# Kernel tuning notes

Measured on AMD Instinct MI355X. Metric: run time of the kernel, lower is better.

Reference implementation:

```python
import jax, jax.numpy as jnp
import numpy as np

NUM_HEADS = 6
KERNEL = 5
EPS = 1e-6


def _neighbor_idx(L, k):
    # NATTEN neighborhood: window start clamped so every query has exactly k neighbors
    starts = jnp.clip(jnp.arange(L) - k // 2, 0, L - k)
    return starts[:, None] + jnp.arange(k)  # [L, k]


def ada_rmsnorm(x, scale, w1, b1, w2, b2):
    # x: [B,C,D,H,W]; RMS over spatial dims, gamma from channel means via small MLP
    rms = jnp.sqrt(jnp.mean(x * x, axis=(2, 3, 4), keepdims=True) + EPS)
    xn = x / rms
    stats = jnp.mean(x, axis=(2, 3, 4))                 # [B,C]
    h = jax.nn.relu(stats @ w1.T + b1)                  # [B,2C]
    gamma = jax.nn.sigmoid(h @ w2.T + b2)               # [B,C]
    return xn * (scale * gamma[:, :, None, None, None])


def reference(x, scale1, n1_w1, n1_b1, n1_w2, n1_b2,
              qkv_w, qkv_b, proj_w, proj_b,
              scale2, n2_w1, n2_b1, n2_w2, n2_b2,
              mlp_w1, mlp_b1, mlp_w2, mlp_b2):
    B, C, D, H, W = x.shape
    nh_, k_ = NUM_HEADS, KERNEL
    hd = C // nh_
    K3 = k_ ** 3

    # --- norm1 + neighborhood attention ---
    h = ada_rmsnorm(x, scale1, n1_w1, n1_b1, n1_w2, n1_b2)
    t = jnp.transpose(h, (0, 2, 3, 4, 1))               # [B,D,H,W,C]
    qkv = t @ qkv_w.T + qkv_b                           # [B,D,H,W,3C]
    q, k, v = jnp.split(qkv, 3, axis=-1)
    q = q.reshape(B, D, H, W, nh_, hd)
    k = k.reshape(B, D, H, W, nh_, hd)
    v = v.reshape(B, D, H, W, nh_, hd)

    iD = _neighbor_idx(D, k_)
    iH = _neighbor_idx(H, k_)
    iW = _neighbor_idx(W, k_)
    nd = iD[:, None, None, :, None, None]               # [D,1,1,k,1,1]
    nhh = iH[None, :, None, None, :, None]              # [1,H,1,1,k,1]
    nw = iW[None, None, :, None, None, :]               # [1,1,W,1,1,k]

    k_nb = k[:, nd, nhh, nw].reshape(B, D, H, W, K3, nh_, hd)
    v_nb = v[:, nd, nhh, nw].reshape(B, D, H, W, K3, nh_, hd)

    scale_qk = hd ** -0.5
    scores = jnp.einsum('bdhwnc,bdhwknc->bdhwnk', q, k_nb) * scale_qk  # [B,D,H,W,heads,K3]
    p = jax.nn.softmax(scores, axis=-1)
    o = jnp.einsum('bdhwnk,bdhwknc->bdhwnc', p, v_nb).reshape(B, D, H, W, C)
    o = o @ proj_w.T + proj_b                            # output projection
    x = x + jnp.transpose(o, (0, 4, 1, 2, 3))

    # --- norm2 + 1x1-conv MLP (GELU exact) ---
    h2 = ada_rmsnorm(x, scale2, n2_w1, n2_b1, n2_w2, n2_b2)
    m = jnp.einsum('oc,bcdhw->bodhw', mlp_w1, h2) + mlp_b1[None, :, None, None, None]
    m = jax.nn.gelu(m, approximate=False)
    m = jnp.einsum('oc,bcdhw->bodhw', mlp_w2, m) + mlp_b2[None, :, None, None, None]
    return x + m


def setup_inputs() -> dict:
    key = jax.random.key(0)
    ks = jax.random.split(key, 16)
    B, C, D, H, W = 1, 192, 16, 16, 16
    hid = 2 * C
    mlp_h = int(4.0 * C)
    s = 0.02
    inp = {
        'x': jax.random.normal(ks[0], (B, C, D, H, W), jnp.float32),
        'scale1': jnp.ones((1, C, 1, 1, 1), jnp.float32),
        'n1_w1': jax.random.normal(ks[1], (hid, C), jnp.float32) * s,
        'n1_b1': jnp.zeros((hid,), jnp.float32),
        'n1_w2': jax.random.normal(ks[2], (C, hid), jnp.float32) * s,
        'n1_b2': jnp.zeros((C,), jnp.float32),
        'qkv_w': jax.random.normal(ks[3], (3 * C, C), jnp.float32) * s,
        'qkv_b': jnp.zeros((3 * C,), jnp.float32),
        'proj_w': jax.random.normal(ks[4], (C, C), jnp.float32) * s,
        'proj_b': jnp.zeros((C,), jnp.float32),
        'scale2': jnp.ones((1, C, 1, 1, 1), jnp.float32),
        'n2_w1': jax.random.normal(ks[5], (hid, C), jnp.float32) * s,
        'n2_b1': jnp.zeros((hid,), jnp.float32),
        'n2_w2': jax.random.normal(ks[6], (C, hid), jnp.float32) * s,
        'n2_b2': jnp.zeros((C,), jnp.float32),
        'mlp_w1': jax.random.normal(ks[7], (mlp_h, C), jnp.float32) * s,
        'mlp_b1': jnp.zeros((mlp_h,), jnp.float32),
        'mlp_w2': jax.random.normal(ks[8], (C, mlp_h), jnp.float32) * s,
        'mlp_b2': jnp.zeros((C,), jnp.float32),
    }
    return inp
```

## Files before the change

kernel.cpp:

```cpp
#include <hip/hip_runtime.h>
#include <hip/hip_bf16.h>
#include <cmath>


#define NPOS 4096
#define C_CH 192

typedef __bf16 bf16x8 __attribute__((ext_vector_type(8)));
typedef __bf16 bf16x4 __attribute__((ext_vector_type(4)));
typedef float  f32x4  __attribute__((ext_vector_type(4)));

__global__ __launch_bounds__(256) void prep_kernel(
    const float* __restrict__ s0, const float* __restrict__ s1,
    const float* __restrict__ s2, const float* __restrict__ s3,
    __bf16* __restrict__ d0, __bf16* __restrict__ d1,
    __bf16* __restrict__ d2, __bf16* __restrict__ d3,
    const float* __restrict__ x, float* __restrict__ sums, float* __restrict__ sumsq)
{
    int b = blockIdx.x;
    if (b < 432) {
        const float* src; __bf16* dst; int base;
        if (b < 108)      { src = s0; dst = d0; base = b; }
        else if (b < 144) { src = s1; dst = d1; base = b - 108; }
        else if (b < 288) { src = s2; dst = d2; base = b - 144; }
        else              { src = s3; dst = d3; base = b - 288; }
        int i = (base * 256 + threadIdx.x) * 4;
        float4 v = *(const float4*)(src + i);
        bf16x4 o = { (__bf16)v.x, (__bf16)v.y, (__bf16)v.z, (__bf16)v.w };
        *(bf16x4*)(dst + i) = o;
        return;
    }
    int c = b - 432;
    const float4* xc = (const float4*)(x + (size_t)c * NPOS);
    float a = 0.f, a2 = 0.f;
    for (int i = threadIdx.x; i < NPOS / 4; i += 256) {
        float4 v = xc[i];
        a  += v.x + v.y + v.z + v.w;
        a2 += v.x * v.x + v.y * v.y + v.z * v.z + v.w * v.w;
    }
    #pragma unroll
    for (int off = 32; off > 0; off >>= 1) {
        a  += __shfl_down(a, off);
        a2 += __shfl_down(a2, off);
    }
    __shared__ float ls[4], ls2[4];
    int wid = threadIdx.x >> 6;
    if ((threadIdx.x & 63) == 0) { ls[wid] = a; ls2[wid] = a2; }
    __syncthreads();
    if (threadIdx.x == 0) {
        float t = 0.f, t2 = 0.f;
        #pragma unroll
        for (int w = 0; w < 4; w++) { t += ls[w]; t2 += ls2[w]; }
        sums[c] = t; sumsq[c] = t2;
    }
}

__global__ __launch_bounds__(256) void stats_kernel(
    const float* __restrict__ x, float* __restrict__ sums, float* __restrict__ sumsq)
{
    int c = blockIdx.x;
    const float4* xc = (const float4*)(x + (size_t)c * NPOS);
    float a = 0.f, a2 = 0.f;
    for (int i = threadIdx.x; i < NPOS / 4; i += 256) {
        float4 v = xc[i];
        a  += v.x + v.y + v.z + v.w;
        a2 += v.x * v.x + v.y * v.y + v.z * v.z + v.w * v.w;
    }
    #pragma unroll
    for (int off = 32; off > 0; off >>= 1) {
        a  += __shfl_down(a, off);
        a2 += __shfl_down(a2, off);
    }
    __shared__ float ls[4], ls2[4];
    int wid = threadIdx.x >> 6;
    if ((threadIdx.x & 63) == 0) { ls[wid] = a; ls2[wid] = a2; }
    __syncthreads();
    if (threadIdx.x == 0) {
        float t = 0.f, t2 = 0.f;
        #pragma unroll
        for (int w = 0; w < 4; w++) { t += ls[w]; t2 += ls2[w]; }
        sums[c] = t; sumsq[c] = t2;
    }
}

__global__ __launch_bounds__(256) void convx_kernel(
    const float* __restrict__ x,
    const float* __restrict__ sums, const float* __restrict__ sumsq,
    const float* __restrict__ scale,
    const float* __restrict__ w1, const float* __restrict__ b1,
    const float* __restrict__ w2, const float* __restrict__ b2,
    __bf16* __restrict__ xb)
{
    __shared__ float stats[C_CH];
    __shared__ float h[384];
    __shared__ float gsl[C_CH];
    __shared__ float lds[192 * 65];
    int t = threadIdx.x;

    if (t < C_CH) stats[t] = sums[t] * (1.0f / (float)NPOS);
    __syncthreads();
    for (int j = t; j < 384; j += 256) {
        float acc = b1[j];
        const float* wr = w1 + (size_t)j * C_CH;
        #pragma unroll 4
        for (int c = 0; c < C_CH; c += 4) {
            float4 w4 = *(const float4*)(wr + c);
            acc += w4.x * stats[c] + w4.y * stats[c + 1] + w4.z * stats[c + 2] + w4.w * stats[c + 3];
        }
        h[j] = fmaxf(acc, 0.0f);
    }
    __syncthreads();
    if (t < C_CH) {
        float acc = b2[t];
        const float* wr = w2 + (size_t)t * 384;
        #pragma unroll 4
        for (int j = 0; j < 384; j += 4) {
            float4 w4 = *(const float4*)(wr + j);
            acc += w4.x * h[j] + w4.y * h[j + 1] + w4.z * h[j + 2] + w4.w * h[j + 3];
        }
        float g = 1.0f / (1.0f + __expf(-acc));
        float rms = sqrtf(sumsq[t] * (1.0f / (float)NPOS) + 1e-6f);
        gsl[t] = scale[t] * g / rms;
    }
    __syncthreads();

    int p0 = blockIdx.x * 64;
    for (int idx = t; idx < 192 * 16; idx += 256) {
        int row = idx >> 4, p4 = idx & 15;
        float4 v = *(const float4*)(x + (size_t)row * NPOS + p0 + p4 * 4);
        float g = gsl[row];
        lds[row * 65 + p4 * 4 + 0] = v.x * g;
        lds[row * 65 + p4 * 4 + 1] = v.y * g;
        lds[row * 65 + p4 * 4 + 2] = v.z * g;
        lds[row * 65 + p4 * 4 + 3] = v.w * g;
    }
    __syncthreads();
    for (int idx = t; idx < 48 * 64; idx += 256) {
        int c4 = idx >> 6, p = idx & 63;
        bf16x4 o;
        #pragma unroll
        for (int j = 0; j < 4; j++) o[j] = (__bf16)lds[(c4 * 4 + j) * 65 + p];
        *(bf16x4*)(xb + (size_t)(p0 + p) * 192 + c4 * 4) = o;
    }
}

template <int K, int EPI, int CFG>
__global__ __launch_bounds__(256) void mfma_gemm(
    const __bf16* __restrict__ W, const float* __restrict__ bias,
    const __bf16* __restrict__ X, void* __restrict__ out,
    const float* __restrict__ resid, int M,
    __bf16* __restrict__ out_kv)
{
    constexpr int MT = 2;
    constexpr int NT = (CFG == 1) ? 2 : 1;
    constexpr int BM = (CFG == 1) ? 64 : 32;
    constexpr int BN = 64;
    int lane = threadIdx.x & 63;
    int wv   = threadIdx.x >> 6;
    int r16  = lane & 15;
    int quad = lane >> 4;
    int wvm = (CFG == 1) ? (wv >> 1) : 0;
    int wvn = (CFG == 1) ? (wv & 1) : wv;
    int mBase = blockIdx.y * BM + wvm * 32;
    int nBase = blockIdx.x * BN + wvn * (NT * 16);

    f32x4 acc[MT][NT];
    #pragma unroll
    for (int i = 0; i < MT; i++)
        #pragma unroll
        for (int j = 0; j < NT; j++)
            acc[i][j] = (f32x4){0.f, 0.f, 0.f, 0.f};

    const __bf16* wp = W + (size_t)(mBase + r16) * K + quad * 8;
    const __bf16* xp = X + (size_t)(nBase + r16) * K + quad * 8;

    #pragma unroll 6
    for (int ks = 0; ks < K / 32; ks++) {
        bf16x8 a[MT], b[NT];
        #pragma unroll
        for (int rt = 0; rt < MT; rt++)
            a[rt] = *(const bf16x8*)(wp + (size_t)rt * 16 * K + ks * 32);
        #pragma unroll
        for (int ct = 0; ct < NT; ct++)
            b[ct] = *(const bf16x8*)(xp + (size_t)ct * 16 * K + ks * 32);
        #pragma unroll
        for (int rt = 0; rt < MT; rt++)
            #pragma unroll
            for (int ct = 0; ct < NT; ct++)
                acc[rt][ct] = __builtin_amdgcn_mfma_f32_16x16x32_bf16(a[rt], b[ct], acc[rt][ct], 0, 0, 0);
    }

    #pragma unroll
    for (int rt = 0; rt < MT; rt++) {
        int m0 = mBase + rt * 16 + quad * 4;
        float b0 = bias[m0], b1 = bias[m0 + 1], b2 = bias[m0 + 2], b3 = bias[m0 + 3];
        #pragma unroll
        for (int ct = 0; ct < NT; ct++) {
            int n = nBase + ct * 16 + r16;
            f32x4 a4 = acc[rt][ct];
            float g0 = a4[0] + b0, g1 = a4[1] + b1, g2 = a4[2] + b2, g3 = a4[3] + b3;
            if (EPI == 0) {
                int sect = m0 / 192;
                int o0 = m0 - sect * 192;
                if (sect == 0) {
                    const float qs = 0.17677669529663687f;
                    *(float4*)((float*)out + (size_t)n * 192 + o0) =
                        make_float4(g0 * qs, g1 * qs, g2 * qs, g3 * qs);
                } else {
                    bf16x4 v = { (__bf16)g0, (__bf16)g1, (__bf16)g2, (__bf16)g3 };
                    *(bf16x4*)(out_kv + (size_t)n * 384 + (sect - 1) * 192 + o0) = v;
                }
            } else if (EPI == 2) {
                float* o = (float*)out;
                size_t i0 = (size_t)m0 * NPOS + n;
                o[i0]            = g0 + resid[i0];
                o[i0 + NPOS]     = g1 + resid[i0 + NPOS];
                o[i0 + 2 * NPOS] = g2 + resid[i0 + 2 * NPOS];
                o[i0 + 3 * NPOS] = g3 + resid[i0 + 3 * NPOS];
            } else {
                bf16x4 v;
                v[0] = (__bf16)(0.5f * g0 * (1.0f + erff(g0 * 0.7071067811865475f)));
                v[1] = (__bf16)(0.5f * g1 * (1.0f + erff(g1 * 0.7071067811865475f)));
                v[2] = (__bf16)(0.5f * g2 * (1.0f + erff(g2 * 0.7071067811865475f)));
                v[3] = (__bf16)(0.5f * g3 * (1.0f + erff(g3 * 0.7071067811865475f)));
                *(bf16x4*)((__bf16*)out + (size_t)n * M + m0) = v;
            }
        }
    }
}

__global__ __launch_bounds__(256) void attn_kernel(
    const float* __restrict__ q, const __bf16* __restrict__ kv, __bf16* __restrict__ o)
{
    int t = threadIdx.x;
    int pairIdx = blockIdx.x * 8 + (t >> 5);
    int sg   = (t >> 3) & 3;
    int lane = t & 7;
    int pos = pairIdx / 6;
    int head = pairIdx - pos * 6;
    int wq = pos & 15;
    int hq = (pos >> 4) & 15;
    int dq = pos >> 8;
    int d0 = min(max(dq - 2, 0), 11);
    int h0 = min(max(hq - 2, 0), 11);
    int w0 = min(max(wq - 2, 0), 11);

    const __bf16* kvb = kv + head * 32 + lane * 4;
    float4 q4 = *(const float4*)(q + (size_t)pos * 192 + head * 32 + lane * 4);

    float l = 0.0f;
    float4 acc = make_float4(0.f, 0.f, 0.f, 0.f);

    for (int dh = sg; dh < 25; dh += 4) {
        int di = dh / 5;
        int hi = dh - di * 5;
        int np0 = (d0 + di) * 256 + (h0 + hi) * 16 + w0;
        const __bf16* p = kvb + (size_t)np0 * 384;
        #pragma unroll
        for (int wi = 0; wi < 5; wi++) {
            uint2 kk = *(const uint2*)p;
            uint2 vv = *(const uint2*)(p + 192);
            float k0 = __uint_as_float(kk.x << 16);
            float k1 = __uint_as_float(kk.x & 0xFFFF0000u);
            float k2 = __uint_as_float(kk.y << 16);
            float k3 = __uint_as_float(kk.y & 0xFFFF0000u);
            float s = q4.x * k0 + q4.y * k1 + q4.z * k2 + q4.w * k3;
            s += __shfl_xor(s, 1);
            s += __shfl_xor(s, 2);
            s += __shfl_xor(s, 4);
            float pr = __expf(s);
            l += pr;
            acc.x += pr * __uint_as_float(vv.x << 16);
            acc.y += pr * __uint_as_float(vv.x & 0xFFFF0000u);
            acc.z += pr * __uint_as_float(vv.y << 16);
            acc.w += pr * __uint_as_float(vv.y & 0xFFFF0000u);
            p += 384;
        }
    }

    #pragma unroll
    for (int off = 8; off <= 16; off <<= 1) {
        l     += __shfl_xor(l, off);
        acc.x += __shfl_xor(acc.x, off);
        acc.y += __shfl_xor(acc.y, off);
        acc.z += __shfl_xor(acc.z, off);
        acc.w += __shfl_xor(acc.w, off);
    }

    if (sg == 0) {
        float rl = 1.0f / l;
        bf16x4 ov = { (__bf16)(acc.x * rl), (__bf16)(acc.y * rl),
                      (__bf16)(acc.z * rl), (__bf16)(acc.w * rl) };
        *(bf16x4*)(o + (size_t)pos * 192 + head * 32 + lane * 4) = ov;
    }
}

extern "C" void kernel_launch(void* const* d_in, const int* in_sizes, int n_in,
                              void* d_out, int out_size, void* d_ws, size_t ws_size,
                              hipStream_t stream)
{
    const float* x      = (const float*)d_in[0];
    const float* scale1 = (const float*)d_in[1];
    const float* n1_w1  = (const float*)d_in[2];
    const float* n1_b1  = (const float*)d_in[3];
    const float* n1_w2  = (const float*)d_in[4];
    const float* n1_b2  = (const float*)d_in[5];
    const float* qkv_w  = (const float*)d_in[6];
    const float* qkv_b  = (const float*)d_in[7];
    const float* proj_w = (const float*)d_in[8];
    const float* proj_b = (const float*)d_in[9];
    const float* scale2 = (const float*)d_in[10];
    const float* n2_w1  = (const float*)d_in[11];
    const float* n2_b1  = (const float*)d_in[12];
    const float* n2_w2  = (const float*)d_in[13];
    const float* n2_b2  = (const float*)d_in[14];
    const float* mlp_w1 = (const float*)d_in[15];
    const float* mlp_b1 = (const float*)d_in[16];
    const float* mlp_w2 = (const float*)d_in[17];
    const float* mlp_b2 = (const float*)d_in[18];

    float* ws = (float*)d_ws;
    float*  q_buf  = ws;
    __bf16* kv_buf = (__bf16*)(ws + 786432);
    __bf16* m_buf  = (__bf16*)ws;
    __bf16* xb     = (__bf16*)(ws + 2359296);
    __bf16* o_attn = (__bf16*)(ws + 2752512);
    __bf16* qkv_wb = (__bf16*)(ws + 3145728);
    __bf16* proj_wb = qkv_wb + 110592;
    __bf16* m1_wb   = proj_wb + 36864;
    __bf16* m2_wb   = m1_wb + 147456;
    float*  sums   = ws + 3366912;
    float*  sumsq  = sums + 192;

    float* x2 = (float*)d_out;

    prep_kernel<<<624, 256, 0, stream>>>(qkv_w, proj_w, mlp_w1, mlp_w2,
                                         qkv_wb, proj_wb, m1_wb, m2_wb,
                                         x, sums, sumsq);
    convx_kernel<<<64, 256, 0, stream>>>(x, sums, sumsq, scale1,
                                         n1_w1, n1_b1, n1_w2, n1_b2, xb);
    mfma_gemm<192, 0, 1><<<dim3(64, 9), 256, 0, stream>>>(qkv_wb, qkv_b, xb, (void*)q_buf, nullptr, 576, kv_buf);
    attn_kernel<<<3072, 256, 0, stream>>>(q_buf, kv_buf, o_attn);
    mfma_gemm<192, 2, 2><<<dim3(64, 6), 256, 0, stream>>>(proj_wb, proj_b, o_attn, (void*)x2, x, 192, nullptr);
    stats_kernel<<<192, 256, 0, stream>>>(x2, sums, sumsq);
    convx_kernel<<<64, 256, 0, stream>>>(x2, sums, sumsq, scale2,
                                         n2_w1, n2_b1, n2_w2, n2_b2, xb);
    mfma_gemm<192, 3, 1><<<dim3(64, 12), 256, 0, stream>>>(m1_wb, mlp_b1, xb, (void*)m_buf, nullptr, 768, nullptr);
    mfma_gemm<768, 2, 2><<<dim3(64, 6), 256, 0, stream>>>(m2_wb, mlp_b2, m_buf, (void*)x2, x2, 192, nullptr);
}
```

Before: 230.1 us.

## Stage GEMM tiles through LDS and store K/V in fp32

Replaces the register-direct MFMA GEMM with an LDS-staged version. Each block cooperatively loads a padded 64x192 slice of both operands into shared memory and four waves compute 32x32 sub-tiles from it. This raises operand reuse and uses 64-row M tiles everywhere, which halves the block count for the projection and second MLP GEMMs. Separately, K and V are now written and read as fp32 rather than bf16, dropping the unpack arithmetic in attention at the cost of doubling the K/V memory footprint and load traffic. The LDS loop has no double buffering, so global loads and MFMA work are not overlapped.

```diff
diff --git a/kernel.cpp b/kernel.cpp
--- a/kernel.cpp
+++ b/kernel.cpp
@@ -144,59 +144,66 @@
     }
 }
 
-template <int K, int EPI, int CFG>
-__global__ __launch_bounds__(256) void mfma_gemm(
+template <int K, int EPI>
+__global__ __launch_bounds__(256) void gemm_lds(
     const __bf16* __restrict__ W, const float* __restrict__ bias,
     const __bf16* __restrict__ X, void* __restrict__ out,
     const float* __restrict__ resid, int M,
-    __bf16* __restrict__ out_kv)
-{
-    constexpr int MT = 2;
-    constexpr int NT = (CFG == 1) ? 2 : 1;
-    constexpr int BM = (CFG == 1) ? 64 : 32;
-    constexpr int BN = 64;
-    int lane = threadIdx.x & 63;
-    int wv   = threadIdx.x >> 6;
+    float* __restrict__ out_kv)
+{
+    constexpr int KC  = 192;
+    constexpr int LDA = 200;
+    __shared__ __bf16 al[64 * LDA];
+    __shared__ __bf16 bl[64 * LDA];
+    int t    = threadIdx.x;
+    int lane = t & 63;
+    int wv   = t >> 6;
     int r16  = lane & 15;
     int quad = lane >> 4;
-    int wvm = (CFG == 1) ? (wv >> 1) : 0;
-    int wvn = (CFG == 1) ? (wv & 1) : wv;
-    int mBase = blockIdx.y * BM + wvm * 32;
-    int nBase = blockIdx.x * BN + wvn * (NT * 16);
-
-    f32x4 acc[MT][NT];
-    #pragma unroll
-    for (int i = 0; i < MT; i++)
-        #pragma unroll
-        for (int j = 0; j < NT; j++)
+    int wvm  = wv >> 1;
+    int wvn  = wv & 1;
+    int mBase = blockIdx.y * 64;
+    int nBase = blockIdx.x * 64;
+
+    f32x4 acc[2][2];
+    #pragma unroll
+    for (int i = 0; i < 2; i++)
+        #pragma unroll
+        for (int j = 0; j < 2; j++)
             acc[i][j] = (f32x4){0.f, 0.f, 0.f, 0.f};
 
-    const __bf16* wp = W + (size_t)(mBase + r16) * K + quad * 8;
-    const __bf16* xp = X + (size_t)(nBase + r16) * K + quad * 8;
-
-    #pragma unroll 6
-    for (int ks = 0; ks < K / 32; ks++) {
-        bf16x8 a[MT], b[NT];
-        #pragma unroll
-        for (int rt = 0; rt < MT; rt++)
-            a[rt] = *(const bf16x8*)(wp + (size_t)rt * 16 * K + ks * 32);
-        #pragma unroll
-        for (int ct = 0; ct < NT; ct++)
-            b[ct] = *(const bf16x8*)(xp + (size_t)ct * 16 * K + ks * 32);
-        #pragma unroll
-        for (int rt = 0; rt < MT; rt++)
-            #pragma unroll
-            for (int ct = 0; ct < NT; ct++)
-                acc[rt][ct] = __builtin_amdgcn_mfma_f32_16x16x32_bf16(a[rt], b[ct], acc[rt][ct], 0, 0, 0);
-    }
-
-    #pragma unroll
-    for (int rt = 0; rt < MT; rt++) {
-        int m0 = mBase + rt * 16 + quad * 4;
+    for (int k0 = 0; k0 < K; k0 += KC) {
+        #pragma unroll
+        for (int it = 0; it < 6; it++) {
+            int c = it * 256 + t;
+            int row = c / 24, off = c - row * 24;
+            bf16x8 va = *(const bf16x8*)(W + (size_t)(mBase + row) * K + k0 + off * 8);
+            *(bf16x8*)(al + row * LDA + off * 8) = va;
+            bf16x8 vb = *(const bf16x8*)(X + (size_t)(nBase + row) * K + k0 + off * 8);
+            *(bf16x8*)(bl + row * LDA + off * 8) = vb;
+        }
+        __syncthreads();
+        #pragma unroll
+        for (int ks = 0; ks < KC / 32; ks++) {
+            bf16x8 a0 = *(const bf16x8*)(al + (wvm * 32 + r16) * LDA + ks * 32 + quad * 8);
+            bf16x8 a1 = *(const bf16x8*)(al + (wvm * 32 + 16 + r16) * LDA + ks * 32 + quad * 8);
+            bf16x8 b0 = *(const bf16x8*)(bl + (wvn * 32 + r16) * LDA + ks * 32 + quad * 8);
+            bf16x8 b1 = *(const bf16x8*)(bl + (wvn * 32 + 16 + r16) * LDA + ks * 32 + quad * 8);
+            acc[0][0] = __builtin_amdgcn_mfma_f32_16x16x32_bf16(a0, b0, acc[0][0], 0, 0, 0);
+            acc[0][1] = __builtin_amdgcn_mfma_f32_16x16x32_bf16(a0, b1, acc[0][1], 0, 0, 0);
+            acc[1][0] = __builtin_amdgcn_mfma_f32_16x16x32_bf16(a1, b0, acc[1][0], 0, 0, 0);
+            acc[1][1] = __builtin_amdgcn_mfma_f32_16x16x32_bf16(a1, b1, acc[1][1], 0, 0, 0);
+        }
+        __syncthreads();
+    }
+
+    #pragma unroll
+    for (int rt = 0; rt < 2; rt++) {
+        int m0 = mBase + wvm * 32 + rt * 16 + quad * 4;
         float b0 = bias[m0], b1 = bias[m0 + 1], b2 = bias[m0 + 2], b3 = bias[m0 + 3];
         #pragma unroll
-        for (int ct = 0; ct < NT; ct++) {
-            int n = nBase + ct * 16 + r16;
+        for (int ct = 0; ct < 2; ct++) {
+            int n = nBase + wvn * 32 + ct * 16 + r16;
             f32x4 a4 = acc[rt][ct];
             float g0 = a4[0] + b0, g1 = a4[1] + b1, g2 = a4[2] + b2, g3 = a4[3] + b3;
             if (EPI == 0) {
@@ -207,8 +214,8 @@
                     *(float4*)((float*)out + (size_t)n * 192 + o0) =
                         make_float4(g0 * qs, g1 * qs, g2 * qs, g3 * qs);
                 } else {
-                    bf16x4 v = { (__bf16)g0, (__bf16)g1, (__bf16)g2, (__bf16)g3 };
-                    *(bf16x4*)(out_kv + (size_t)n * 384 + (sect - 1) * 192 + o0) = v;
+                    *(float4*)(out_kv + (size_t)n * 384 + (sect - 1) * 192 + o0) =
+                        make_float4(g0, g1, g2, g3);
                 }
             } else if (EPI == 2) {
                 float* o = (float*)out;
@@ -230,7 +237,7 @@
 }
 
 __global__ __launch_bounds__(256) void attn_kernel(
-    const float* __restrict__ q, const __bf16* __restrict__ kv, __bf16* __restrict__ o)
+    const float* __restrict__ q, const float* __restrict__ kv, __bf16* __restrict__ o)
 {
     int t = threadIdx.x;
     int pairIdx = blockIdx.x * 8 + (t >> 5);
@@ -245,7 +252,7 @@
     int h0 = min(max(hq - 2, 0), 11);
     int w0 = min(max(wq - 2, 0), 11);
 
-    const __bf16* kvb = kv + head * 32 + lane * 4;
+    const float* kvb = kv + head * 32 + lane * 4;
     float4 q4 = *(const float4*)(q + (size_t)pos * 192 + head * 32 + lane * 4);
 
     float l = 0.0f;
@@ -255,25 +262,21 @@
         int di = dh / 5;
         int hi = dh - di * 5;
         int np0 = (d0 + di) * 256 + (h0 + hi) * 16 + w0;
-        const __bf16* p = kvb + (size_t)np0 * 384;
+        const float* p = kvb + (size_t)np0 * 384;
         #pragma unroll
         for (int wi = 0; wi < 5; wi++) {
-            uint2 kk = *(const uint2*)p;
-            uint2 vv = *(const uint2*)(p + 192);
-            float k0 = __uint_as_float(kk.x << 16);
-            float k1 = __uint_as_float(kk.x & 0xFFFF0000u);
-            float k2 = __uint_as_float(kk.y << 16);
-            float k3 = __uint_as_float(kk.y & 0xFFFF0000u);
-            float s = q4.x * k0 + q4.y * k1 + q4.z * k2 + q4.w * k3;
+            float4 k4 = *(const float4*)p;
+            float4 v4 = *(const float4*)(p + 192);
+            float s = q4.x * k4.x + q4.y * k4.y + q4.z * k4.z + q4.w * k4.w;
             s += __shfl_xor(s, 1);
             s += __shfl_xor(s, 2);
             s += __shfl_xor(s, 4);
             float pr = __expf(s);
             l += pr;
-            acc.x += pr * __uint_as_float(vv.x << 16);
-            acc.y += pr * __uint_as_float(vv.x & 0xFFFF0000u);
-            acc.z += pr * __uint_as_float(vv.y << 16);
-            acc.w += pr * __uint_as_float(vv.y & 0xFFFF0000u);
+            acc.x += pr * v4.x;
+            acc.y += pr * v4.y;
+            acc.z += pr * v4.z;
+            acc.w += pr * v4.w;
             p += 384;
         }
     }
@@ -321,7 +324,7 @@
 
     float* ws = (float*)d_ws;
     float*  q_buf  = ws;
-    __bf16* kv_buf = (__bf16*)(ws + 786432);
+    float*  kv_buf = ws + 786432;
     __bf16* m_buf  = (__bf16*)ws;
     __bf16* xb     = (__bf16*)(ws + 2359296);
     __bf16* o_attn = (__bf16*)(ws + 2752512);
@@ -339,12 +342,12 @@
                                          x, sums, sumsq);
     convx_kernel<<<64, 256, 0, stream>>>(x, sums, sumsq, scale1,
                                          n1_w1, n1_b1, n1_w2, n1_b2, xb);
-    mfma_gemm<192, 0, 1><<<dim3(64, 9), 256, 0, stream>>>(qkv_wb, qkv_b, xb, (void*)q_buf, nullptr, 576, kv_buf);
+    gemm_lds<192, 0><<<dim3(64, 9), 256, 0, stream>>>(qkv_wb, qkv_b, xb, (void*)q_buf, nullptr, 576, kv_buf);
     attn_kernel<<<3072, 256, 0, stream>>>(q_buf, kv_buf, o_attn);
-    mfma_gemm<192, 2, 2><<<dim3(64, 6), 256, 0, stream>>>(proj_wb, proj_b, o_attn, (void*)x2, x, 192, nullptr);
+    gemm_lds<192, 2><<<dim3(64, 3), 256, 0, stream>>>(proj_wb, proj_b, o_attn, (void*)x2, x, 192, nullptr);
     stats_kernel<<<192, 256, 0, stream>>>(x2, sums, sumsq);
     convx_kernel<<<64, 256, 0, stream>>>(x2, sums, sumsq, scale2,
                                          n2_w1, n2_b1, n2_w2, n2_b2, xb);
-    mfma_gemm<192, 3, 1><<<dim3(64, 12), 256, 0, stream>>>(m1_wb, mlp_b1, xb, (void*)m_buf, nullptr, 768, nullptr);
-    mfma_gemm<768, 2, 2><<<dim3(64, 6), 256, 0, stream>>>(m2_wb, mlp_b2, m_buf, (void*)x2, x2, 192, nullptr);
-}
+    gemm_lds<192, 3><<<dim3(64, 12), 256, 0, stream>>>(m1_wb, mlp_b1, xb, (void*)m_buf, nullptr, 768, nullptr);
+    gemm_lds<768, 2><<<dim3(64, 3), 256, 0, stream>>>(m2_wb, mlp_b2, m_buf, (void*)x2, x2, 192, nullptr);
+}
```

After: 204.1 us. -11.3%, faster.
